# Kernel tuning notes

Hardware: AMD Instinct MI355X
Metric: run time of the kernel (lower is better)

The kernel has to match this reference:

```python
import jax, jax.numpy as jnp
import numpy as np

N_HEADS = 16
HEAD_DIM = 128  # d_model // n_heads


def rope(x):
    # x: [B, H, T, D]. Matches the torch module: interleaved even/odd split,
    # then concat([x1*cos - x2*sin, x1*sin + x2*cos], axis=-1).
    T, D = x.shape[2], x.shape[3]
    inv_freq = 1.0 / (10000.0 ** (jnp.arange(0, D, 2, dtype=x.dtype) / D))  # [D/2]
    freqs = jnp.arange(T, dtype=x.dtype)[:, None] * inv_freq[None, :]       # [T, D/2]
    sin, cos = jnp.sin(freqs), jnp.cos(freqs)                               # [T, D/2]
    x1, x2 = x[..., ::2], x[..., 1::2]                                      # [B,H,T,D/2]
    return jnp.concatenate([x1 * cos - x2 * sin, x1 * sin + x2 * cos], axis=-1)


def setup_inputs() -> dict:
    key = jax.random.key(0)
    ks = jax.random.split(key, 5)
    B, T, C = 2, 2048, 2048
    scale = 1.0 / np.sqrt(C)
    return {
        "x": jax.random.normal(ks[0], (B, T, C), dtype=jnp.float32),
        "W_qkv": jax.random.normal(ks[1], (3 * C, C), dtype=jnp.float32) * scale,
        "b_qkv": jnp.zeros((3 * C,), dtype=jnp.float32),
        "W_out": jax.random.normal(ks[2], (C, C), dtype=jnp.float32) * scale,
        "b_out": jnp.zeros((C,), dtype=jnp.float32),
    }


def reference(x, W_qkv, b_qkv, W_out, b_out):
    B, T, C = x.shape
    H, D = N_HEADS, HEAD_DIM
    qkv = x @ W_qkv.T + b_qkv                      # [B, T, 3C]
    qkv = qkv.reshape(B, T, 3, H, D)
    q, k, v = qkv[:, :, 0], qkv[:, :, 1], qkv[:, :, 2]  # [B, T, H, D]
    q = rope(jnp.transpose(q, (0, 2, 1, 3)))       # [B, H, T, D]
    k = rope(jnp.transpose(k, (0, 2, 1, 3)))
    v = jnp.transpose(v, (0, 2, 1, 3))
    scores = jnp.einsum("bhqd,bhkd->bhqk", q, k) / jnp.sqrt(jnp.asarray(D, x.dtype))
    causal = jnp.tril(jnp.ones((T, T), dtype=bool))
    scores = jnp.where(causal, scores, jnp.finfo(x.dtype).min)
    attn = jax.nn.softmax(scores, axis=-1)
    out = jnp.einsum("bhqk,bhkd->bhqd", attn, v)   # [B, H, T, D]
    out = jnp.transpose(out, (0, 2, 1, 3)).reshape(B, T, C)
    return out @ W_out.T + b_out
```

## Files before the change

### kernel.cpp

```cpp
#include <hip/hip_runtime.h>
#include <hip/hip_bf16.h>

typedef __attribute__((ext_vector_type(8))) short bf16x8;
typedef __attribute__((ext_vector_type(4))) float f32x4;

#define GLOAD_LDS16(gptr, lptr) \
  __builtin_amdgcn_global_load_lds((const __attribute__((address_space(1))) void*)(gptr), \
                                   (__attribute__((address_space(3))) void*)(lptr), 16, 0, 0)

__device__ __forceinline__ unsigned short f2b(float f) {
  union { float f; unsigned u; } x; x.f = f;
  unsigned r = x.u + 0x7fffu + ((x.u >> 16) & 1u);
  return (unsigned short)(r >> 16);
}
__device__ __forceinline__ float b2f(unsigned short u) {
  union { unsigned u; float f; } x; x.u = ((unsigned)u) << 16;
  return x.f;
}

__global__ void cast_kernel(const float* __restrict__ in, unsigned short* __restrict__ out, int n) {
  const int i = (blockIdx.x * 256 + threadIdx.x) * 4;
  if (i < n) {
    const float4 v = *(const float4*)(in + i);
    ushort4 r;
    r.x = f2b(v.x); r.y = f2b(v.y); r.z = f2b(v.z); r.w = f2b(v.w);
    *(ushort4*)(out + i) = r;
  }
}

template<int OUTF32>
__global__ __launch_bounds__(512, 2)
void gemm256(const unsigned short* __restrict__ A,
             const unsigned short* __restrict__ Bm,
             const float* __restrict__ bias,
             void* __restrict__ Cp,
             int M, int N, int K)
{
  __shared__ __align__(16) char Lds[131072];
  const int t  = threadIdx.x;
  const int l  = t & 63;
  const int w  = t >> 6;
  const int lr = l & 15;
  const int lkb = (l >> 4) << 4;
  const int wr = w >> 2;
  const int wc = w & 3;

  const int nwg = gridDim.x;
  const int wg  = (blockIdx.x & 7) * (nwg >> 3) + (blockIdx.x >> 3);
  const int NBN = N >> 8;
  const int bm = wg / NBN, bn = wg % NBN;

  const int sw3 = (lr & 7) << 4;
  const int ck0 = lkb ^ sw3;
  const int ck1 = (64 | lkb) ^ sw3;

  const int lb0 = t << 4;
  const int lb1 = lb0 + 8192;
  const int d0 = lb0 ^ (((lb0 >> 7) & 7) << 4);
  const int d1 = lb1 ^ (((lb1 >> 7) & 7) << 4);
  const long K2 = (long)K * 2;
  const char* Ab = (const char*)A  + (long)(bm * 256) * K2;
  const char* Bb = (const char*)Bm + (long)(bn * 256) * K2;
  const long s0 = (long)(d0 >> 7) * K2 + (d0 & 127);
  const long s1 = (long)(d1 >> 7) * K2 + (d1 & 127);
  const long hstep = (long)128 * K2;

  auto stageA = [&](int g, int h) {
    char* dst = Lds + (g & 1) * 65536 + h * 16384;
    const char* src = Ab + (long)h * hstep + (long)g * 128;
    GLOAD_LDS16(src + s0, dst + lb0);
    GLOAD_LDS16(src + s1, dst + lb1);
  };
  auto stageB = [&](int g, int h) {
    char* dst = Lds + (g & 1) * 65536 + 32768 + h * 16384;
    const char* src = Bb + (long)h * hstep + (long)g * 128;
    GLOAD_LDS16(src + s0, dst + lb0);
    GLOAD_LDS16(src + s1, dst + lb1);
  };

  f32x4 acc[8][4] = {};
  const int NT = K >> 6;
  const int brow = ((wc & 1) * 64 + lr) << 7;

  bf16x8 af[4][2], blo[2][2], bhi[2][2];

  stageA(0, 0); stageA(0, 1);
  stageB(0, 0); stageB(0, 1);
  stageB(1, 0); stageB(1, 1);
  asm volatile("s_waitcnt vmcnt(4)" ::: "memory");
  __builtin_amdgcn_s_barrier();
  {
    const char* AH0 = Lds + wr * 16384;
    const char* BH0 = Lds + 32768 + (wc >> 1) * 16384;
#pragma unroll
    for (int ni = 0; ni < 2; ++ni) {
      blo[ni][0] = *(const bf16x8*)(BH0 + brow + (ni << 11) + ck0);
      blo[ni][1] = *(const bf16x8*)(BH0 + brow + (ni << 11) + ck1);
    }
#pragma unroll
    for (int mi = 0; mi < 4; ++mi) {
      af[mi][0] = *(const bf16x8*)(AH0 + ((mi * 16 + lr) << 7) + ck0);
      af[mi][1] = *(const bf16x8*)(AH0 + ((mi * 16 + lr) << 7) + ck1);
    }
#pragma unroll
    for (int ni = 0; ni < 2; ++ni) {
      bhi[ni][0] = *(const bf16x8*)(BH0 + brow + ((ni + 2) << 11) + ck0);
      bhi[ni][1] = *(const bf16x8*)(BH0 + brow + ((ni + 2) << 11) + ck1);
    }
  }

  for (int tt = 0; tt < NT; ++tt) {
    const char* SB = Lds + (tt & 1) * 65536;
    const char* AH = SB + wr * 16384;

    if (tt + 1 < NT) { stageA(tt + 1, 0); stageA(tt + 1, 1); }
    __builtin_amdgcn_s_barrier();
    __builtin_amdgcn_sched_barrier(0);
    __builtin_amdgcn_s_setprio(1);
#pragma unroll
    for (int mi = 0; mi < 4; ++mi)
#pragma unroll
      for (int ni = 0; ni < 2; ++ni) {
        acc[mi][ni] = __builtin_amdgcn_mfma_f32_16x16x32_bf16(af[mi][0], blo[ni][0], acc[mi][ni], 0, 0, 0);
        acc[mi][ni] = __builtin_amdgcn_mfma_f32_16x16x32_bf16(af[mi][1], blo[ni][1], acc[mi][ni], 0, 0, 0);
      }
    __builtin_amdgcn_s_setprio(0);
    __builtin_amdgcn_s_barrier();
    __builtin_amdgcn_sched_barrier(0);

    __builtin_amdgcn_s_setprio(1);
#pragma unroll
    for (int mi = 0; mi < 4; ++mi)
#pragma unroll
      for (int ni = 0; ni < 2; ++ni) {
        acc[mi][ni + 2] = __builtin_amdgcn_mfma_f32_16x16x32_bf16(af[mi][0], bhi[ni][0], acc[mi][ni + 2], 0, 0, 0);
        acc[mi][ni + 2] = __builtin_amdgcn_mfma_f32_16x16x32_bf16(af[mi][1], bhi[ni][1], acc[mi][ni + 2], 0, 0, 0);
      }
    __builtin_amdgcn_s_setprio(0);
#pragma unroll
    for (int mi = 0; mi < 4; ++mi) {
      af[mi][0] = *(const bf16x8*)(AH + ((64 + mi * 16 + lr) << 7) + ck0);
      af[mi][1] = *(const bf16x8*)(AH + ((64 + mi * 16 + lr) << 7) + ck1);
    }
    __builtin_amdgcn_s_barrier();
    __builtin_amdgcn_sched_barrier(0);

    asm volatile("s_waitcnt vmcnt(0)" ::: "memory");
    if (tt + 2 < NT) stageB(tt + 2, 0);
    __builtin_amdgcn_s_setprio(1);
#pragma unroll
    for (int mi = 0; mi < 4; ++mi)
#pragma unroll
      for (int ni = 0; ni < 2; ++ni) {
        acc[mi + 4][ni] = __builtin_amdgcn_mfma_f32_16x16x32_bf16(af[mi][0], blo[ni][0], acc[mi + 4][ni], 0, 0, 0);
        acc[mi + 4][ni] = __builtin_amdgcn_mfma_f32_16x16x32_bf16(af[mi][1], blo[ni][1], acc[mi + 4][ni], 0, 0, 0);
      }
    __builtin_amdgcn_s_setprio(0);
    if (tt + 1 < NT) {
      const char* BHn = Lds + ((tt + 1) & 1) * 65536 + 32768 + (wc >> 1) * 16384;
#pragma unroll
      for (int ni = 0; ni < 2; ++ni) {
        blo[ni][0] = *(const bf16x8*)(BHn + brow + (ni << 11) + ck0);
        blo[ni][1] = *(const bf16x8*)(BHn + brow + (ni << 11) + ck1);
      }
    }
    __builtin_amdgcn_s_barrier();
    __builtin_amdgcn_sched_barrier(0);

    if (tt + 2 < NT) stageB(tt + 2, 1);
    __builtin_amdgcn_s_setprio(1);
#pragma unroll
    for (int mi = 0; mi < 4; ++mi)
#pragma unroll
      for (int ni = 0; ni < 2; ++ni) {
        acc[mi + 4][ni + 2] = __builtin_amdgcn_mfma_f32_16x16x32_bf16(af[mi][0], bhi[ni][0], acc[mi + 4][ni + 2], 0, 0, 0);
        acc[mi + 4][ni + 2] = __builtin_amdgcn_mfma_f32_16x16x32_bf16(af[mi][1], bhi[ni][1], acc[mi + 4][ni + 2], 0, 0, 0);
      }
    __builtin_amdgcn_s_setprio(0);
    if (tt + 1 < NT) {
      const char* SBn = Lds + ((tt + 1) & 1) * 65536;
      const char* AHn = SBn + wr * 16384;
      const char* BHn = SBn + 32768 + (wc >> 1) * 16384;
#pragma unroll
      for (int mi = 0; mi < 4; ++mi) {
        af[mi][0] = *(const bf16x8*)(AHn + ((mi * 16 + lr) << 7) + ck0);
        af[mi][1] = *(const bf16x8*)(AHn + ((mi * 16 + lr) << 7) + ck1);
      }
#pragma unroll
      for (int ni = 0; ni < 2; ++ni) {
        bhi[ni][0] = *(const bf16x8*)(BHn + brow + ((ni + 2) << 11) + ck0);
        bhi[ni][1] = *(const bf16x8*)(BHn + brow + ((ni + 2) << 11) + ck1);
      }
    }
    __builtin_amdgcn_s_barrier();
    __builtin_amdgcn_sched_barrier(0);
  }

  const int roff = (l >> 4) << 2;
  const int row0 = bm * 256 + wr * 128 + roff;
  const int col0 = bn * 256 + wc * 64 + lr;
  float bv[4];
#pragma unroll
  for (int ni = 0; ni < 4; ++ni) bv[ni] = bias ? bias[col0 + ni * 16] : 0.0f;
#pragma unroll
  for (int mi = 0; mi < 8; ++mi) {
#pragma unroll
    for (int r = 0; r < 4; ++r) {
      const long rb = (long)(row0 + mi * 16 + r) * N;
#pragma unroll
      for (int ni = 0; ni < 4; ++ni) {
        const float v = acc[mi][ni][r] + bv[ni];
        if (OUTF32) ((float*)Cp)[rb + col0 + ni * 16] = v;
        else ((unsigned short*)Cp)[rb + col0 + ni * 16] = f2b(v);
      }
    }
  }
}

__global__ void prep_kernel(const unsigned short* __restrict__ qkv,
                            unsigned short* __restrict__ Qr,
                            unsigned short* __restrict__ Kr,
                            unsigned short* __restrict__ Vt)
{
  const int T = 2048;
  __shared__ unsigned short ld[128][65];
  const int bh = blockIdx.y, tb = blockIdx.x;
  const int b = bh >> 4, h = bh & 15;
  const int t = threadIdx.x;

#pragma unroll
  for (int i = 0; i < 16; ++i) {
    const int idx = i * 256 + t;
    const int d  = idx & 63;
    const int tt = tb * 64 + (idx >> 6);
    const long base = ((long)(b * T + tt) * 3) * 2048 + h * 128;
    const float inv = exp2f(-(float)d * 0.2076205059304602f);
    const float fr = (float)tt * inv;
    float sn, cs;
    sincosf(fr, &sn, &cs);
    const float q1 = b2f(qkv[base + 2 * d]);
    const float q2 = b2f(qkv[base + 2 * d + 1]);
    const float k1 = b2f(qkv[base + 2048 + 2 * d]);
    const float k2 = b2f(qkv[base + 2048 + 2 * d + 1]);
    const long ob = ((long)bh * T + tt) * 128;
    Qr[ob + d]      = f2b(q1 * cs - q2 * sn);
    Qr[ob + 64 + d] = f2b(q1 * sn + q2 * cs);
    Kr[ob + d]      = f2b(k1 * cs - k2 * sn);
    Kr[ob + 64 + d] = f2b(k1 * sn + k2 * cs);
  }

#pragma unroll
  for (int i = 0; i < 32; ++i) {
    const int idx = i * 256 + t;
    const int d = idx & 127, tr = idx >> 7;
    ld[d][tr] = qkv[((long)(b * T + tb * 64 + tr) * 3 + 2) * 2048 + h * 128 + d];
  }
  __syncthreads();
#pragma unroll
  for (int i = 0; i < 32; ++i) {
    const int idx = i * 256 + t;
    const int tc = idx & 63, dr = idx >> 6;
    Vt[((long)bh * 128 + dr) * T + tb * 64 + tc] = ld[dr][tc];
  }
}

__global__ __launch_bounds__(256)
void attn_fwd(const unsigned short* __restrict__ Q,
              const unsigned short* __restrict__ Kg,
              const unsigned short* __restrict__ Vt,
              unsigned short* __restrict__ O, int T)
{
  __shared__ __align__(16) unsigned short Ks[2][64 * 128];
  __shared__ __align__(16) unsigned short Vs[2][128 * 64];
  __shared__ __align__(16) unsigned short Ps[4][16 * 64];
  const int t = threadIdx.x;
  const int w = t >> 6, l = t & 63;
  const int lr = l & 15;
  const int g16 = (l >> 4) << 4;
  const int sw = (lr & 7) << 4;
  const int bh = blockIdx.x;
  const int qt = (gridDim.y - 1) - blockIdx.y;
  const int q0 = qt * 64 + w * 16;
  const long hbase = (long)bh * T * 128;
  const long hbase2 = hbase * 2;
  const long T2 = (long)T * 2;
  const int roff = (l >> 4) << 2;
  const float C1 = 0.08838834764831845f * 1.4426950408889634f;

  bf16x8 qf[4];
  const unsigned short* Qrow = Q + hbase + (long)(q0 + lr) * 128;
#pragma unroll
  for (int ds = 0; ds < 4; ++ds) qf[ds] = *(const bf16x8*)&Qrow[ds * 32 + (g16 >> 1)];

  f32x4 o[8] = {};
  float m[4]    = {-INFINITY, -INFINITY, -INFINITY, -INFINITY};
  float lsum[4] = {0.f, 0.f, 0.f, 0.f};

  auto stage = [&](int kt, int buf) {
#pragma unroll
    for (int c = 0; c < 4; ++c) {
      const int o2 = t * 16 + c * 4096;
      const int krow = o2 >> 8, kcb = o2 & 255;
      GLOAD_LDS16((const char*)Kg + hbase2 + (long)kt * 16384 + krow * 256 + (kcb ^ ((krow & 7) << 4)),
                  (char*)Ks[buf] + o2);
      const int vrow = o2 >> 7, vcb = o2 & 127;
      GLOAD_LDS16((const char*)Vt + (long)(bh * 128 + vrow) * T2 + (long)kt * 128 + (vcb ^ ((vrow & 7) << 4)),
                  (char*)Vs[buf] + o2);
    }
  };

  const int ntile = qt + 1;
  stage(0, 0);
  __syncthreads();

  for (int kt = 0; kt < ntile; ++kt) {
    const int cur = kt & 1;
    if (kt + 1 < ntile) stage(kt + 1, cur ^ 1);

    const char* KsB = (const char*)Ks[cur];
    const char* VsB = (const char*)Vs[cur];

    f32x4 s[4] = {};
    __builtin_amdgcn_s_setprio(1);
#pragma unroll
    for (int tj = 0; tj < 4; ++tj)
#pragma unroll
      for (int ds = 0; ds < 4; ++ds) {
        bf16x8 kf = *(const bf16x8*)(KsB + (tj * 16 + lr) * 256 + ((ds * 64 + g16) ^ sw));
        s[tj] = __builtin_amdgcn_mfma_f32_16x16x32_bf16(qf[ds], kf, s[tj], 0, 0, 0);
      }
    __builtin_amdgcn_s_setprio(0);

    if (kt == qt) {
#pragma unroll
      for (int tj = 0; tj < 4; ++tj)
#pragma unroll
        for (int j = 0; j < 4; ++j)
          if (kt * 64 + tj * 16 + lr > q0 + roff + j) s[tj][j] = -INFINITY;
    }

    float corr[4];
#pragma unroll
    for (int j = 0; j < 4; ++j) {
      float v = fmaxf(fmaxf(s[0][j], s[1][j]), fmaxf(s[2][j], s[3][j]));
      v = fmaxf(v, __shfl_xor(v, 1, 64));
      v = fmaxf(v, __shfl_xor(v, 2, 64));
      v = fmaxf(v, __shfl_xor(v, 4, 64));
      v = fmaxf(v, __shfl_xor(v, 8, 64));
      const float mn = fmaxf(m[j], v * C1);
      corr[j] = exp2f(m[j] - mn);
      m[j] = mn;
    }
    float rs[4] = {0.f, 0.f, 0.f, 0.f};
#pragma unroll
    for (int tj = 0; tj < 4; ++tj)
#pragma unroll
      for (int j = 0; j < 4; ++j) {
        const float p = exp2f(fmaf(s[tj][j], C1, -m[j]));
        rs[j] += p;
        const int prow = roff + j;
        *(unsigned short*)((char*)Ps[w] + prow * 128 + (((tj * 16 + lr) * 2) ^ ((prow & 7) << 4))) = f2b(p);
      }
#pragma unroll
    for (int j = 0; j < 4; ++j) {
      float v = rs[j];
      v += __shfl_xor(v, 1, 64);
      v += __shfl_xor(v, 2, 64);
      v += __shfl_xor(v, 4, 64);
      v += __shfl_xor(v, 8, 64);
      lsum[j] = lsum[j] * corr[j] + v;
    }
#pragma unroll
    for (int nj = 0; nj < 8; ++nj)
#pragma unroll
      for (int j = 0; j < 4; ++j) o[nj][j] *= corr[j];

    __builtin_amdgcn_s_setprio(1);
#pragma unroll
    for (int ks = 0; ks < 2; ++ks) {
      bf16x8 pf = *(const bf16x8*)((const char*)Ps[w] + lr * 128 + ((ks * 64 + g16) ^ sw));
#pragma unroll
      for (int nj = 0; nj < 8; ++nj) {
        bf16x8 vf = *(const bf16x8*)(VsB + (nj * 16 + lr) * 128 + ((ks * 64 + g16) ^ sw));
        o[nj] = __builtin_amdgcn_mfma_f32_16x16x32_bf16(pf, vf, o[nj], 0, 0, 0);
      }
    }
    __builtin_amdgcn_s_setprio(0);
    __syncthreads();
  }

  float inv[4];
#pragma unroll
  for (int j = 0; j < 4; ++j) inv[j] = 1.0f / lsum[j];
  const int b = bh >> 4, h = bh & 15;
#pragma unroll
  for (int nj = 0; nj < 8; ++nj)
#pragma unroll
    for (int j = 0; j < 4; ++j) {
      const int q = q0 + roff + j;
      const int d = nj * 16 + lr;
      O[(long)(b * T + q) * 2048 + h * 128 + d] = f2b(o[nj][j] * inv[j]);
    }
}

extern "C" void kernel_launch(void* const* d_in, const int* in_sizes, int n_in,
                              void* d_out, int out_size, void* d_ws, size_t ws_size,
                              hipStream_t stream)
{
  const int B = 2, T = 2048, C = 2048;
  const int M = B * T;
  const int N1 = 3 * C;
  const float* x    = (const float*)d_in[0];
  const float* Wqkv = (const float*)d_in[1];
  const float* bqkv = (const float*)d_in[2];
  const float* Wout = (const float*)d_in[3];
  const float* bout = (const float*)d_in[4];
  float* out = (float*)d_out;

  char* p = (char*)d_ws;
  unsigned short* xb    = (unsigned short*)p; p += (size_t)M * C * 2;
  unsigned short* wqkvb = (unsigned short*)p; p += (size_t)N1 * C * 2;
  unsigned short* woutb = (unsigned short*)p; p += (size_t)C * C * 2;
  unsigned short* qkv   = (unsigned short*)p; p += (size_t)M * N1 * 2;
  unsigned short* Qr    = (unsigned short*)p; p += (size_t)M * C * 2;
  unsigned short* Kr    = (unsigned short*)p; p += (size_t)M * C * 2;
  unsigned short* Vt    = (unsigned short*)p; p += (size_t)M * C * 2;
  unsigned short* Ob    = xb;

  cast_kernel<<<M * C / 1024, 256, 0, stream>>>(x, xb, M * C);
  cast_kernel<<<N1 * C / 1024, 256, 0, stream>>>(Wqkv, wqkvb, N1 * C);
  cast_kernel<<<C * C / 1024, 256, 0, stream>>>(Wout, woutb, C * C);

  gemm256<0><<<dim3((M / 256) * (N1 / 256)), 512, 0, stream>>>(xb, wqkvb, bqkv, qkv, M, N1, C);

  prep_kernel<<<dim3(T / 64, 32), 256, 0, stream>>>(qkv, Qr, Kr, Vt);

  attn_fwd<<<dim3(32, T / 64), 256, 0, stream>>>(Qr, Kr, Vt, Ob, T);

  gemm256<1><<<dim3((M / 256) * (C / 256)), 512, 0, stream>>>(Ob, woutb, bout, out, M, C, C);
}
```

Before: 312.0 us.

## Shrink GEMM block tile from 256x256 to 128x256 to raise block count

Halves the M dimension of each GEMM workgroup tile, reducing accumulators, A fragments and the LDS footprint, and doubles the grid for both projection GEMMs. This is meant to fill more CUs, especially for the output projection, which previously launched only 128 blocks. In exchange each B tile is reused across fewer rows, which raises global/LDS traffic per flop.

After: 310.2 us. Within noise of the previous version (-0.6%).

```diff
diff --git a/kernel.cpp b/kernel.cpp
--- a/kernel.cpp
+++ b/kernel.cpp
@@ -30,13 +30,13 @@
 
 template<int OUTF32>
 __global__ __launch_bounds__(512, 2)
-void gemm256(const unsigned short* __restrict__ A,
+void gemm128(const unsigned short* __restrict__ A,
              const unsigned short* __restrict__ Bm,
              const float* __restrict__ bias,
              void* __restrict__ Cp,
              int M, int N, int K)
 {
-  __shared__ __align__(16) char Lds[131072];
+  __shared__ __align__(16) char Lds[98304];
   const int t  = threadIdx.x;
   const int l  = t & 63;
   const int w  = t >> 6;
@@ -54,71 +54,72 @@
   const int ck0 = lkb ^ sw3;
   const int ck1 = (64 | lkb) ^ sw3;
 
-  const int lb0 = t << 4;
-  const int lb1 = lb0 + 8192;
-  const int d0 = lb0 ^ (((lb0 >> 7) & 7) << 4);
-  const int d1 = lb1 ^ (((lb1 >> 7) & 7) << 4);
   const long K2 = (long)K * 2;
-  const char* Ab = (const char*)A  + (long)(bm * 256) * K2;
+  const char* Ab = (const char*)A  + (long)(bm * 128) * K2;
   const char* Bb = (const char*)Bm + (long)(bn * 256) * K2;
-  const long s0 = (long)(d0 >> 7) * K2 + (d0 & 127);
-  const long s1 = (long)(d1 >> 7) * K2 + (d1 & 127);
-  const long hstep = (long)128 * K2;
-
-  auto stageA = [&](int g, int h) {
-    char* dst = Lds + (g & 1) * 65536 + h * 16384;
-    const char* src = Ab + (long)h * hstep + (long)g * 128;
-    GLOAD_LDS16(src + s0, dst + lb0);
-    GLOAD_LDS16(src + s1, dst + lb1);
+
+  auto swzsrc = [&](int lo) -> long {
+    const int d = lo ^ (((lo >> 7) & 7) << 4);
+    return (long)(d >> 7) * K2 + (d & 127);
   };
-  auto stageB = [&](int g, int h) {
-    char* dst = Lds + (g & 1) * 65536 + 32768 + h * 16384;
-    const char* src = Bb + (long)h * hstep + (long)g * 128;
-    GLOAD_LDS16(src + s0, dst + lb0);
-    GLOAD_LDS16(src + s1, dst + lb1);
+  const int t16 = t << 4;
+  const long a0 = swzsrc(t16),          a1 = swzsrc(t16 + 8192);
+  const long b0 = a0,                   b1 = a1;
+  const long b2 = swzsrc(t16 + 16384),  b3 = swzsrc(t16 + 24576);
+
+  auto stageA = [&](int g) {
+    char* dst = Lds + (g & 1) * 49152 + t16;
+    const char* src = Ab + (long)g * 128;
+    GLOAD_LDS16(src + a0, dst);
+    GLOAD_LDS16(src + a1, dst + 8192);
   };
-
-  f32x4 acc[8][4] = {};
+  auto stageB2 = [&](int g, int half) {
+    char* dst = Lds + (g & 1) * 49152 + 16384 + half * 16384 + t16;
+    const char* src = Bb + (long)g * 128;
+    GLOAD_LDS16(src + (half ? b2 : b0), dst);
+    GLOAD_LDS16(src + (half ? b3 : b1), dst + 8192);
+  };
+
+  f32x4 acc[4][4] = {};
   const int NT = K >> 6;
-  const int brow = ((wc & 1) * 64 + lr) << 7;
-
-  bf16x8 af[4][2], blo[2][2], bhi[2][2];
-
-  stageA(0, 0); stageA(0, 1);
-  stageB(0, 0); stageB(0, 1);
-  stageB(1, 0); stageB(1, 1);
+
+  bf16x8 af[2][2], blo[2][2], bhi[2][2];
+
+  stageA(0);
+  stageB2(0, 0); stageB2(0, 1);
+  stageB2(1, 0); stageB2(1, 1);
   asm volatile("s_waitcnt vmcnt(4)" ::: "memory");
   __builtin_amdgcn_s_barrier();
   {
-    const char* AH0 = Lds + wr * 16384;
-    const char* BH0 = Lds + 32768 + (wc >> 1) * 16384;
+    const char* AH0 = Lds + wr * 8192;
+    const char* BH0 = Lds + 16384 + wc * 8192;
 #pragma unroll
     for (int ni = 0; ni < 2; ++ni) {
-      blo[ni][0] = *(const bf16x8*)(BH0 + brow + (ni << 11) + ck0);
-      blo[ni][1] = *(const bf16x8*)(BH0 + brow + (ni << 11) + ck1);
-    }
-#pragma unroll
-    for (int mi = 0; mi < 4; ++mi) {
+      blo[ni][0] = *(const bf16x8*)(BH0 + ((ni * 16 + lr) << 7) + ck0);
+      blo[ni][1] = *(const bf16x8*)(BH0 + ((ni * 16 + lr) << 7) + ck1);
+    }
+#pragma unroll
+    for (int mi = 0; mi < 2; ++mi) {
       af[mi][0] = *(const bf16x8*)(AH0 + ((mi * 16 + lr) << 7) + ck0);
       af[mi][1] = *(const bf16x8*)(AH0 + ((mi * 16 + lr) << 7) + ck1);
     }
 #pragma unroll
     for (int ni = 0; ni < 2; ++ni) {
-      bhi[ni][0] = *(const bf16x8*)(BH0 + brow + ((ni + 2) << 11) + ck0);
-      bhi[ni][1] = *(const bf16x8*)(BH0 + brow + ((ni + 2) << 11) + ck1);
+      bhi[ni][0] = *(const bf16x8*)(BH0 + (((ni + 2) * 16 + lr) << 7) + ck0);
+      bhi[ni][1] = *(const bf16x8*)(BH0 + (((ni + 2) * 16 + lr) << 7) + ck1);
     }
   }
 
   for (int tt = 0; tt < NT; ++tt) {
-    const char* SB = Lds + (tt & 1) * 65536;
-    const char* AH = SB + wr * 16384;
-
-    if (tt + 1 < NT) { stageA(tt + 1, 0); stageA(tt + 1, 1); }
+    const char* SB = Lds + (tt & 1) * 49152;
+    const char* AH = SB + wr * 8192;
+
+    if (tt + 1 < NT) stageA(tt + 1);
     __builtin_amdgcn_s_barrier();
     __builtin_amdgcn_sched_barrier(0);
     __builtin_amdgcn_s_setprio(1);
 #pragma unroll
-    for (int mi = 0; mi < 4; ++mi)
+    for (int mi = 0; mi < 2; ++mi)
 #pragma unroll
       for (int ni = 0; ni < 2; ++ni) {
         acc[mi][ni] = __builtin_amdgcn_mfma_f32_16x16x32_bf16(af[mi][0], blo[ni][0], acc[mi][ni], 0, 0, 0);
@@ -130,7 +131,7 @@
 
     __builtin_amdgcn_s_setprio(1);
 #pragma unroll
-    for (int mi = 0; mi < 4; ++mi)
+    for (int mi = 0; mi < 2; ++mi)
 #pragma unroll
       for (int ni = 0; ni < 2; ++ni) {
         acc[mi][ni + 2] = __builtin_amdgcn_mfma_f32_16x16x32_bf16(af[mi][0], bhi[ni][0], acc[mi][ni + 2], 0, 0, 0);
@@ -138,58 +139,58 @@
       }
     __builtin_amdgcn_s_setprio(0);
 #pragma unroll
-    for (int mi = 0; mi < 4; ++mi) {
-      af[mi][0] = *(const bf16x8*)(AH + ((64 + mi * 16 + lr) << 7) + ck0);
-      af[mi][1] = *(const bf16x8*)(AH + ((64 + mi * 16 + lr) << 7) + ck1);
+    for (int mi = 0; mi < 2; ++mi) {
+      af[mi][0] = *(const bf16x8*)(AH + (((mi + 2) * 16 + lr) << 7) + ck0);
+      af[mi][1] = *(const bf16x8*)(AH + (((mi + 2) * 16 + lr) << 7) + ck1);
     }
     __builtin_amdgcn_s_barrier();
     __builtin_amdgcn_sched_barrier(0);
 
     asm volatile("s_waitcnt vmcnt(0)" ::: "memory");
-    if (tt + 2 < NT) stageB(tt + 2, 0);
-    __builtin_amdgcn_s_setprio(1);
-#pragma unroll
-    for (int mi = 0; mi < 4; ++mi)
-#pragma unroll
-      for (int ni = 0; ni < 2; ++ni) {
-        acc[mi + 4][ni] = __builtin_amdgcn_mfma_f32_16x16x32_bf16(af[mi][0], blo[ni][0], acc[mi + 4][ni], 0, 0, 0);
-        acc[mi + 4][ni] = __builtin_amdgcn_mfma_f32_16x16x32_bf16(af[mi][1], blo[ni][1], acc[mi + 4][ni], 0, 0, 0);
+    if (tt + 2 < NT) stageB2(tt + 2, 0);
+    __builtin_amdgcn_s_setprio(1);
+#pragma unroll
+    for (int mi = 0; mi < 2; ++mi)
+#pragma unroll
+      for (int ni = 0; ni < 2; ++ni) {
+        acc[mi + 2][ni] = __builtin_amdgcn_mfma_f32_16x16x32_bf16(af[mi][0], blo[ni][0], acc[mi + 2][ni], 0, 0, 0);
+        acc[mi + 2][ni] = __builtin_amdgcn_mfma_f32_16x16x32_bf16(af[mi][1], blo[ni][1], acc[mi + 2][ni], 0, 0, 0);
       }
     __builtin_amdgcn_s_setprio(0);
     if (tt + 1 < NT) {
-      const char* BHn = Lds + ((tt + 1) & 1) * 65536 + 32768 + (wc >> 1) * 16384;
-#pragma unroll
-      for (int ni = 0; ni < 2; ++ni) {
-        blo[ni][0] = *(const bf16x8*)(BHn + brow + (ni << 11) + ck0);
-        blo[ni][1] = *(const bf16x8*)(BHn + brow + (ni << 11) + ck1);
+      const char* BHn = Lds + ((tt + 1) & 1) * 49152 + 16384 + wc * 8192;
+#pragma unroll
+      for (int ni = 0; ni < 2; ++ni) {
+        blo[ni][0] = *(const bf16x8*)(BHn + ((ni * 16 + lr) << 7) + ck0);
+        blo[ni][1] = *(const bf16x8*)(BHn + ((ni * 16 + lr) << 7) + ck1);
       }
     }
     __builtin_amdgcn_s_barrier();
     __builtin_amdgcn_sched_barrier(0);
 
-    if (tt + 2 < NT) stageB(tt + 2, 1);
-    __builtin_amdgcn_s_setprio(1);
-#pragma unroll
-    for (int mi = 0; mi < 4; ++mi)
-#pragma unroll
-      for (int ni = 0; ni < 2; ++ni) {
-        acc[mi + 4][ni + 2] = __builtin_amdgcn_mfma_f32_16x16x32_bf16(af[mi][0], bhi[ni][0], acc[mi + 4][ni + 2], 0, 0, 0);
-        acc[mi + 4][ni + 2] = __builtin_amdgcn_mfma_f32_16x16x32_bf16(af[mi][1], bhi[ni][1], acc[mi + 4][ni + 2], 0, 0, 0);
+    if (tt + 2 < NT) stageB2(tt + 2, 1);
+    __builtin_amdgcn_s_setprio(1);
+#pragma unroll
+    for (int mi = 0; mi < 2; ++mi)
+#pragma unroll
+      for (int ni = 0; ni < 2; ++ni) {
+        acc[mi + 2][ni + 2] = __builtin_amdgcn_mfma_f32_16x16x32_bf16(af[mi][0], bhi[ni][0], acc[mi + 2][ni + 2], 0, 0, 0);
+        acc[mi + 2][ni + 2] = __builtin_amdgcn_mfma_f32_16x16x32_bf16(af[mi][1], bhi[ni][1], acc[mi + 2][ni + 2], 0, 0, 0);
       }
     __builtin_amdgcn_s_setprio(0);
     if (tt + 1 < NT) {
-      const char* SBn = Lds + ((tt + 1) & 1) * 65536;
-      const char* AHn = SBn + wr * 16384;
-      const char* BHn = SBn + 32768 + (wc >> 1) * 16384;
-#pragma unroll
-      for (int mi = 0; mi < 4; ++mi) {
+      const char* SBn = Lds + ((tt + 1) & 1) * 49152;
+      const char* AHn = SBn + wr * 8192;
+      const char* BHn = SBn + 16384 + wc * 8192;
+#pragma unroll
+      for (int mi = 0; mi < 2; ++mi) {
         af[mi][0] = *(const bf16x8*)(AHn + ((mi * 16 + lr) << 7) + ck0);
         af[mi][1] = *(const bf16x8*)(AHn + ((mi * 16 + lr) << 7) + ck1);
       }
 #pragma unroll
       for (int ni = 0; ni < 2; ++ni) {
-        bhi[ni][0] = *(const bf16x8*)(BHn + brow + ((ni + 2) << 11) + ck0);
-        bhi[ni][1] = *(const bf16x8*)(BHn + brow + ((ni + 2) << 11) + ck1);
+        bhi[ni][0] = *(const bf16x8*)(BHn + (((ni + 2) * 16 + lr) << 7) + ck0);
+        bhi[ni][1] = *(const bf16x8*)(BHn + (((ni + 2) * 16 + lr) << 7) + ck1);
       }
     }
     __builtin_amdgcn_s_barrier();
@@ -197,13 +198,13 @@
   }
 
   const int roff = (l >> 4) << 2;
-  const int row0 = bm * 256 + wr * 128 + roff;
+  const int row0 = bm * 128 + wr * 64 + roff;
   const int col0 = bn * 256 + wc * 64 + lr;
   float bv[4];
 #pragma unroll
   for (int ni = 0; ni < 4; ++ni) bv[ni] = bias ? bias[col0 + ni * 16] : 0.0f;
 #pragma unroll
-  for (int mi = 0; mi < 8; ++mi) {
+  for (int mi = 0; mi < 4; ++mi) {
 #pragma unroll
     for (int r = 0; r < 4; ++r) {
       const long rb = (long)(row0 + mi * 16 + r) * N;
@@ -431,11 +432,11 @@
   cast_kernel<<<N1 * C / 1024, 256, 0, stream>>>(Wqkv, wqkvb, N1 * C);
   cast_kernel<<<C * C / 1024, 256, 0, stream>>>(Wout, woutb, C * C);
 
-  gemm256<0><<<dim3((M / 256) * (N1 / 256)), 512, 0, stream>>>(xb, wqkvb, bqkv, qkv, M, N1, C);
+  gemm128<0><<<dim3((M / 128) * (N1 / 256)), 512, 0, stream>>>(xb, wqkvb, bqkv, qkv, M, N1, C);
 
   prep_kernel<<<dim3(T / 64, 32), 256, 0, stream>>>(qkv, Qr, Kr, Vt);
 
   attn_fwd<<<dim3(32, T / 64), 256, 0, stream>>>(Qr, Kr, Vt, Ob, T);
 
-  gemm256<1><<<dim3((M / 256) * (C / 256)), 512, 0, stream>>>(Ob, woutb, bout, out, M, C, C);
-}
+  gemm128<1><<<dim3((M / 128) * (C / 256)), 512, 0, stream>>>(Ob, woutb, bout, out, M, C, C);
+}
```
